# Performance work log

Measured on AMD Instinct MI355X. Metric: run time of the kernel, lower is better.

The kernel has to match this reference:

```python
import math
import jax, jax.numpy as jnp
import numpy as np

L, H, C, HS = 12, 12, 768, 64
V, BS = 50304, 1024
B, T = 2, 1024
FINAL_TH = 0.0005
MIN_KEEP = 64


def _layernorm(x, w, b):
    m = x.mean(-1, keepdims=True)
    v = ((x - m) ** 2).mean(-1, keepdims=True)
    return (x - m) * jax.lax.rsqrt(v + 1e-5) * w + b


def setup_inputs() -> dict:
    key = jax.random.key(0)
    ks = jax.random.split(key, 12)
    std = 0.02
    inp = {
        "idx": jax.random.randint(ks[0], (B, T), 0, V),
        "targets": jax.random.randint(ks[1], (B, T), 0, V),
        # embeddings (wte is tied with lm_head)
        "wte": jax.random.normal(ks[2], (V, C), jnp.float32) * std,
        "wpe": jax.random.normal(ks[3], (BS, C), jnp.float32) * std,
        # stacked per-layer params (leading dim L) -- weights stored (in, out)
        "ln1_w": jnp.ones((L, C), jnp.float32),
        "ln1_b": jnp.zeros((L, C), jnp.float32),
        "attn_w": jax.random.normal(ks[4], (L, C, 3 * C), jnp.float32) * std,
        "attn_b": jnp.zeros((L, 3 * C), jnp.float32),
        "proj_w": jax.random.normal(ks[5], (L, C, C), jnp.float32) * std,
        "proj_b": jnp.zeros((L, C), jnp.float32),
        "ln2_w": jnp.ones((L, C), jnp.float32),
        "ln2_b": jnp.zeros((L, C), jnp.float32),
        "fc_w": jax.random.normal(ks[6], (L, C, 4 * C), jnp.float32) * std,
        "fc_b": jnp.zeros((L, 4 * C), jnp.float32),
        "mlp_w": jax.random.normal(ks[7], (L, 4 * C, C), jnp.float32) * std,
        "mlp_b": jnp.zeros((L, C), jnp.float32),
        # learned thresholds: (layer_idx+1)/n_layer * final_token_threshold
        "thresholds": (jnp.arange(1, L + 1, dtype=jnp.float32) / L) * FINAL_TH,
        "lnf_w": jnp.ones((C,), jnp.float32),
        "lnf_b": jnp.zeros((C,), jnp.float32),
    }
    return inp


def _forward(idx, targets, wte, wpe, ln1_w, ln1_b, attn_w, attn_b, proj_w, proj_b,
             ln2_w, ln2_b, fc_w, fc_b, mlp_w, mlp_b, thresholds, lnf_w, lnf_b):
    Bv, Tv = idx.shape
    x = wte[idx] + wpe[:Tv]  # (B,T,C); dropout=0 -> identity
    causal = jnp.tril(jnp.ones((Tv, Tv), bool))
    protected = jnp.zeros((Bv, Tv), jnp.float32).at[:, -MIN_KEEP:].set(1.0)
    am0 = jnp.ones((Bv, Tv), jnp.float32)

    def block(carry, p):
        x, am = carry
        l1w, l1b, aw, ab, pw, pb, l2w, l2b, fw, fb, mw, mb, th = p
        h = _layernorm(x, l1w, l1b)
        qkv = h @ aw + ab  # (B,T,3C)
        q, k, v = jnp.split(qkv, 3, axis=-1)
        q = q.reshape(Bv, Tv, H, HS).transpose(0, 2, 1, 3)  # (B,H,T,hs)
        k = k.reshape(Bv, Tv, H, HS).transpose(0, 2, 1, 3)
        v = v.reshape(Bv, Tv, H, HS).transpose(0, 2, 1, 3)
        att = jnp.einsum('bhqd,bhkd->bhqk', q, k) / math.sqrt(HS)
        keym = am[:, None, None, :] > 0
        att = jnp.where(causal[None, None] & keym, att, -jnp.inf)
        att = jax.nn.softmax(att, axis=-1)  # attn_dropout=0
        y = jnp.einsum('bhqk,bhkd->bhqd', att, v)
        y = y.transpose(0, 2, 1, 3).reshape(Bv, Tv, C) @ pw + pb  # resid_dropout=0
        x = x + y
        imp = att.mean(axis=(1, 2))  # (B,T): mean over heads then queries
        pm = (imp >= th).astype(x.dtype)  # hard mask
        pm = jnp.where(protected > 0, 1.0, pm)
        cm = am * pm
        x = x * cm[..., None]
        h2 = _layernorm(x, l2w, l2b)
        x = x + (jax.nn.gelu(h2 @ fw + fb, approximate=False) @ mw + mb)
        return (x, cm), None

    params = (ln1_w, ln1_b, attn_w, attn_b, proj_w, proj_b,
              ln2_w, ln2_b, fc_w, fc_b, mlp_w, mlp_b, thresholds)
    (x, am), _ = jax.lax.scan(block, (x, am0), params)
    x = _layernorm(x, lnf_w, lnf_b)
    logits = x @ wte.T  # tied lm_head
    logp = jax.nn.log_softmax(logits, axis=-1)
    nll = -jnp.take_along_axis(logp, targets[..., None], axis=-1)[..., 0]
    valid = targets != -1  # ignore_index=-1
    loss = jnp.where(valid, nll, 0.0).sum() / valid.sum()
    # hard masking => pruning loss is 0, loss == lm_loss
    return logits, loss


def reference(idx, targets, wte, wpe, ln1_w, ln1_b, attn_w, attn_b, proj_w, proj_b,
              ln2_w, ln2_b, fc_w, fc_b, mlp_w, mlp_b, thresholds, lnf_w, lnf_b):
    return _forward(idx, targets, wte, wpe, ln1_w, ln1_b, attn_w, attn_b,
                    proj_w, proj_b, ln2_w, ln2_b, fc_w, fc_b, mlp_w, mlp_b,
                    thresholds, lnf_w, lnf_b)
```

## Files before the change

kernel.cpp:

```cpp
#include <hip/hip_runtime.h>
#include <math.h>


#define LNUM 12
#define HNUM 12
#define CDIM 768
#define VDIM 50304
#define TDIM 1024
#define BDIM 2
#define NROWS 2048
#define LDSK 40

typedef unsigned short u16;
typedef __attribute__((ext_vector_type(8))) short short8;
typedef __attribute__((ext_vector_type(4))) float floatx4;
typedef __attribute__((ext_vector_type(4))) unsigned short ushort4v;
typedef __attribute__((ext_vector_type(8))) unsigned short ushort8v;

__device__ __forceinline__ unsigned short f2bf_rne(float f) {
  unsigned u = __float_as_uint(f);
  u += 0x7fff + ((u >> 16) & 1);
  return (unsigned short)(u >> 16);
}
__device__ __forceinline__ float bf2f(unsigned short h) {
  return __uint_as_float(((unsigned)h) << 16);
}

__device__ __forceinline__ void gload16(const void* g, void* l) {
  __builtin_amdgcn_global_load_lds(
      (const __attribute__((address_space(1))) unsigned int*)g,
      (__attribute__((address_space(3))) unsigned int*)l, 16, 0, 0);
}

__device__ __forceinline__ float bred(float v, int op) {
  __shared__ float red[256];
  const int tid = threadIdx.x;
  red[tid] = v;
  __syncthreads();
#pragma unroll
  for (int s = 128; s > 0; s >>= 1) {
    if (tid < s) {
      float o = red[tid + s];
      red[tid] = op ? fmaxf(red[tid], o) : (red[tid] + o);
    }
    __syncthreads();
  }
  float r = red[0];
  __syncthreads();
  return r;
}

__global__ void k_embed(const int* __restrict__ idx, const float* __restrict__ wte,
                        const float* __restrict__ wpe, float* __restrict__ x,
                        float* __restrict__ am) {
  const int row = blockIdx.x;
  const int t = row & (TDIM - 1);
  const long tok = idx[row];
  const float* src = wte + tok * CDIM;
  const float* pp = wpe + (long)t * CDIM;
  float* dst = x + (long)row * CDIM;
  for (int c = threadIdx.x; c < CDIM; c += 256) dst[c] = src[c] + pp[c];
  if (threadIdx.x == 0) am[row] = 1.0f;
}

__global__ void k_layernorm(const float* __restrict__ in, const float* __restrict__ w,
                            const float* __restrict__ b, float* __restrict__ out) {
  const long row = blockIdx.x;
  const int tid = threadIdx.x;
  const float* xr = in + row * CDIM;
  float v0 = xr[tid], v1 = xr[tid + 256], v2 = xr[tid + 512];
  float mean = bred(v0 + v1 + v2, 0) * (1.0f / CDIM);
  float d0 = v0 - mean, d1 = v1 - mean, d2 = v2 - mean;
  float var = bred(d0 * d0 + d1 * d1 + d2 * d2, 0) * (1.0f / CDIM);
  float inv = 1.0f / sqrtf(var + 1e-5f);
  float* orow = out + row * CDIM;
  orow[tid]       = d0 * inv * w[tid]       + b[tid];
  orow[tid + 256] = d1 * inv * w[tid + 256] + b[tid + 256];
  orow[tid + 512] = d2 * inv * w[tid + 512] + b[tid + 512];
}

__global__ void k_layernorm_sp(const float* __restrict__ in, const float* __restrict__ w,
                               const float* __restrict__ b, u16* __restrict__ ohi,
                               u16* __restrict__ olo) {
  const long row = blockIdx.x;
  const int tid = threadIdx.x;
  const float* xr = in + row * CDIM;
  float v0 = xr[tid], v1 = xr[tid + 256], v2 = xr[tid + 512];
  float mean = bred(v0 + v1 + v2, 0) * (1.0f / CDIM);
  float d0 = v0 - mean, d1 = v1 - mean, d2 = v2 - mean;
  float var = bred(d0 * d0 + d1 * d1 + d2 * d2, 0) * (1.0f / CDIM);
  float inv = 1.0f / sqrtf(var + 1e-5f);
  float o0 = d0 * inv * w[tid]       + b[tid];
  float o1 = d1 * inv * w[tid + 256] + b[tid + 256];
  float o2 = d2 * inv * w[tid + 512] + b[tid + 512];
  u16* hr = ohi + row * CDIM;
  u16* lr = olo + row * CDIM;
  u16 h0 = f2bf_rne(o0), h1 = f2bf_rne(o1), h2 = f2bf_rne(o2);
  hr[tid] = h0;       lr[tid] = f2bf_rne(o0 - bf2f(h0));
  hr[tid + 256] = h1; lr[tid + 256] = f2bf_rne(o1 - bf2f(h1));
  hr[tid + 512] = h2; lr[tid + 512] = f2bf_rne(o2 - bf2f(h2));
}

__global__ void k_wsplit(const float* __restrict__ W, u16* __restrict__ Whi,
                         u16* __restrict__ Wlo, int K, int N, long wstride, long ostride) {
  W += blockIdx.z * wstride;
  Whi += blockIdx.z * ostride;
  Wlo += blockIdx.z * ostride;
  const int n0 = blockIdx.x << 6, k0 = blockIdx.y << 6;
  __shared__ float t[64][65];
  const int tid = threadIdx.x;
  const int cr = tid >> 4;
  const int cc = (tid & 15) << 2;
#pragma unroll
  for (int it = 0; it < 4; ++it) {
    const int r = cr + it * 16;
    float4 v = *(const float4*)(W + (long)(k0 + r) * N + n0 + cc);
    t[r][cc] = v.x; t[r][cc + 1] = v.y; t[r][cc + 2] = v.z; t[r][cc + 3] = v.w;
  }
  __syncthreads();
#pragma unroll
  for (int it = 0; it < 4; ++it) {
    const int n = cr + it * 16;
    ushort4v hv, lv;
#pragma unroll
    for (int j = 0; j < 4; ++j) {
      float f = t[cc + j][n];
      u16 hh = f2bf_rne(f);
      hv[j] = hh;
      lv[j] = f2bf_rne(f - bf2f(hh));
    }
    *(ushort4v*)&Whi[(long)(n0 + n) * K + k0 + cc] = hv;
    *(ushort4v*)&Wlo[(long)(n0 + n) * K + k0 + cc] = lv;
  }
}

__global__ void k_cvt_hi(const float* __restrict__ A, u16* __restrict__ O, long n) {
  long i = ((long)blockIdx.x * 256 + threadIdx.x) * 8;
  if (i >= n) return;
  float4 a = *(const float4*)(A + i);
  float4 b = *(const float4*)(A + i + 4);
  ushort8v o;
  o[0] = f2bf_rne(a.x); o[1] = f2bf_rne(a.y); o[2] = f2bf_rne(a.z); o[3] = f2bf_rne(a.w);
  o[4] = f2bf_rne(b.x); o[5] = f2bf_rne(b.y); o[6] = f2bf_rne(b.z); o[7] = f2bf_rne(b.w);
  *(ushort8v*)&O[i] = o;
}

template <int BT, int ACT, int OSPLIT>
__global__ __launch_bounds__(256) void k_gemm(
    const float* __restrict__ A, const float* __restrict__ B,
    const float* __restrict__ bias, float* __restrict__ C,
    u16* __restrict__ Ohi, u16* __restrict__ Olo,
    int K, int lda, int ldb, int ldc,
    long sAb, long sAh, long sBb, long sBh, long sCb, long sCh,
    int Hb, float alpha, int beta) {
  const int bid = blockIdx.z;
  const int bb = bid / Hb, hh = bid - bb * Hb;
  A += bb * sAb + hh * sAh;
  B += bb * sBb + hh * sBh;
  C += bb * sCb + hh * sCh;
  if (OSPLIT) { Ohi += bb * sCb + hh * sCh; Olo += bb * sCb + hh * sCh; }
  const int m0 = blockIdx.y << 6, n0 = blockIdx.x << 6;
  __shared__ float As[16][68];
  __shared__ float Bs[16][68];
  const int tid = threadIdx.x;
  const int r0 = (tid >> 4) << 2;
  const int c0 = (tid & 15) << 2;
  const int lr = tid >> 2;
  const int lk = (tid & 3) << 2;
  const int bk = tid >> 4;
  const int bn = (tid & 15) << 2;
  float acc[4][4] = {{0.f, 0.f, 0.f, 0.f}, {0.f, 0.f, 0.f, 0.f},
                     {0.f, 0.f, 0.f, 0.f}, {0.f, 0.f, 0.f, 0.f}};
  for (int k0 = 0; k0 < K; k0 += 16) {
    float4 av = *(const float4*)(A + (long)(m0 + lr) * lda + (k0 + lk));
    As[lk][lr] = av.x; As[lk + 1][lr] = av.y; As[lk + 2][lr] = av.z; As[lk + 3][lr] = av.w;
    if (BT) {
      float4 bv = *(const float4*)(B + (long)(n0 + lr) * ldb + (k0 + lk));
      Bs[lk][lr] = bv.x; Bs[lk + 1][lr] = bv.y; Bs[lk + 2][lr] = bv.z; Bs[lk + 3][lr] = bv.w;
    } else {
      *(float4*)&Bs[bk][bn] = *(const float4*)(B + (long)(k0 + bk) * ldb + (n0 + bn));
    }
    __syncthreads();
#pragma unroll
    for (int kk = 0; kk < 16; ++kk) {
      float4 a = *(const float4*)&As[kk][r0];
      float4 bv = *(const float4*)&Bs[kk][c0];
      acc[0][0] += a.x * bv.x; acc[0][1] += a.x * bv.y; acc[0][2] += a.x * bv.z; acc[0][3] += a.x * bv.w;
      acc[1][0] += a.y * bv.x; acc[1][1] += a.y * bv.y; acc[1][2] += a.y * bv.z; acc[1][3] += a.y * bv.w;
      acc[2][0] += a.z * bv.x; acc[2][1] += a.z * bv.y; acc[2][2] += a.z * bv.z; acc[2][3] += a.z * bv.w;
      acc[3][0] += a.w * bv.x; acc[3][1] += a.w * bv.y; acc[3][2] += a.w * bv.z; acc[3][3] += a.w * bv.w;
    }
    __syncthreads();
  }
  float4 bs4 = make_float4(0.f, 0.f, 0.f, 0.f);
  if (bias) bs4 = *(const float4*)(bias + n0 + c0);
#pragma unroll
  for (int i = 0; i < 4; ++i) {
    float* cp = C + (long)(m0 + r0 + i) * ldc + (n0 + c0);
    float4 prev = make_float4(0.f, 0.f, 0.f, 0.f);
    if (beta) prev = *(const float4*)cp;
    float4 o;
    o.x = prev.x + alpha * acc[i][0] + bs4.x;
    o.y = prev.y + alpha * acc[i][1] + bs4.y;
    o.z = prev.z + alpha * acc[i][2] + bs4.z;
    o.w = prev.w + alpha * acc[i][3] + bs4.w;
    if (ACT == 1) {
      o.x = 0.5f * o.x * (1.0f + erff(o.x * 0.70710678118654752f));
      o.y = 0.5f * o.y * (1.0f + erff(o.y * 0.70710678118654752f));
      o.z = 0.5f * o.z * (1.0f + erff(o.z * 0.70710678118654752f));
      o.w = 0.5f * o.w * (1.0f + erff(o.w * 0.70710678118654752f));
    }
    if (OSPLIT) {
      ushort4v hv, lv;
      hv[0] = f2bf_rne(o.x); lv[0] = f2bf_rne(o.x - bf2f(hv[0]));
      hv[1] = f2bf_rne(o.y); lv[1] = f2bf_rne(o.y - bf2f(hv[1]));
      hv[2] = f2bf_rne(o.z); lv[2] = f2bf_rne(o.z - bf2f(hv[2]));
      hv[3] = f2bf_rne(o.w); lv[3] = f2bf_rne(o.w - bf2f(hv[3]));
      *(ushort4v*)(Ohi + (long)(m0 + r0 + i) * ldc + (n0 + c0)) = hv;
      *(ushort4v*)(Olo + (long)(m0 + r0 + i) * ldc + (n0 + c0)) = lv;
    } else {
      *(float4*)cp = o;
    }
  }
}

template <int TERMS, int ACT, int OUTMODE, int GS>
__global__ __launch_bounds__(256) void k_gemm_bt(
    const u16* __restrict__ Ahi, const u16* __restrict__ Alo,
    const u16* __restrict__ Bhi, const u16* __restrict__ Blo,
    const float* __restrict__ bias, float* __restrict__ C,
    u16* __restrict__ Ohi, u16* __restrict__ Olo,
    int K, int lda, int ldb, int ldc,
    long sAb, long sAh, long sBb, long sBh, long sCb, long sCh,
    int Hb, float alpha, int beta) {
  const int bz = blockIdx.z;
  const int bb = bz / Hb, hh = bz - bb * Hb;
  Ahi += bb * sAb + hh * sAh;
  Bhi += bb * sBb + hh * sBh;
  if (TERMS > 1) {
    Alo += bb * sAb + hh * sAh;
    Blo += bb * sBb + hh * sBh;
  }
  if (OUTMODE != 1) C += bb * sCb + hh * sCh;
  if (OUTMODE >= 1) { Ohi += bb * sCb + hh * sCh; Olo += bb * sCb + hh * sCh; }
  const int m0 = (GS ? blockIdx.x : blockIdx.y) << 7;
  const int n0 = (GS ? blockIdx.y : blockIdx.x) << 7;
  __shared__ u16 sm[(TERMS > 1 ? 4 : 2) * 4096];
  u16* sAhi = sm;
  u16* sAlo = sm + 4096;
  u16* sBhi = sm + (TERMS > 1 ? 2 : 1) * 4096;
  u16* sBlo = sBhi + 4096;
  const int tid = threadIdx.x;
  const int lane = tid & 63, wave = tid >> 6;
  const int wm = (wave & 1) << 6, wn = (wave >> 1) << 6;
  const int fr = lane & 15, fk = (lane >> 4) << 3;
  const int sr = lane >> 2;
  const int sc = (lane & 3) << 3;
  const long arow = (long)(m0 + wave * 32 + sr);
  const long brow = (long)(n0 + wave * 32 + sr);
  const int lbase = wave * 1024;

  floatx4 acc[4][4];
#pragma unroll
  for (int i = 0; i < 4; ++i)
#pragma unroll
    for (int j = 0; j < 4; ++j) acc[i][j] = (floatx4)(0.0f);

  for (int k0 = 0; k0 < K; k0 += 32) {
    {
      const u16* ga = Ahi + arow * lda + k0 + sc;
      const u16* gb = Bhi + brow * ldb + k0 + sc;
      gload16(ga, &sAhi[lbase]);
      gload16(ga + (long)16 * lda, &sAhi[lbase + 512]);
      gload16(gb, &sBhi[lbase]);
      gload16(gb + (long)16 * ldb, &sBhi[lbase + 512]);
      if (TERMS > 1) {
        const u16* ga2 = Alo + arow * lda + k0 + sc;
        const u16* gb2 = Blo + brow * ldb + k0 + sc;
        gload16(ga2, &sAlo[lbase]);
        gload16(ga2 + (long)16 * lda, &sAlo[lbase + 512]);
        gload16(gb2, &sBlo[lbase]);
        gload16(gb2 + (long)16 * ldb, &sBlo[lbase + 512]);
      }
    }
    __syncthreads();
    short8 ah[4], bh[4], al[4], bl[4];
#pragma unroll
    for (int i = 0; i < 4; ++i) {
      ah[i] = *(const short8*)&sAhi[(wm + i * 16 + fr) * 32 + fk];
      bh[i] = *(const short8*)&sBhi[(wn + i * 16 + fr) * 32 + fk];
      if (TERMS > 1) {
        al[i] = *(const short8*)&sAlo[(wm + i * 16 + fr) * 32 + fk];
        bl[i] = *(const short8*)&sBlo[(wn + i * 16 + fr) * 32 + fk];
      }
    }
#pragma unroll
    for (int i = 0; i < 4; ++i)
#pragma unroll
      for (int j = 0; j < 4; ++j) {
        acc[i][j] = __builtin_amdgcn_mfma_f32_16x16x32_bf16(ah[i], bh[j], acc[i][j], 0, 0, 0);
        if (TERMS > 1) {
          acc[i][j] = __builtin_amdgcn_mfma_f32_16x16x32_bf16(ah[i], bl[j], acc[i][j], 0, 0, 0);
          acc[i][j] = __builtin_amdgcn_mfma_f32_16x16x32_bf16(al[i], bh[j], acc[i][j], 0, 0, 0);
        }
      }
    __syncthreads();
  }
  const int er = (lane >> 4) << 2, ec = lane & 15;
#pragma unroll
  for (int j = 0; j < 4; ++j) {
    const int col = n0 + wn + j * 16 + ec;
    const float bsv = bias ? bias[col] : 0.0f;
#pragma unroll
    for (int i = 0; i < 4; ++i) {
      const long rbase = (long)(m0 + wm + i * 16 + er);
#pragma unroll
      for (int r = 0; r < 4; ++r) {
        const long off = (rbase + r) * ldc + col;
        float o = alpha * acc[i][j][r] + bsv;
        if (beta) o += C[off];
        if (ACT == 1) o = 0.5f * o * (1.0f + erff(o * 0.70710678118654752f));
        if (OUTMODE != 1) C[off] = o;
        if (OUTMODE >= 1) {
          u16 hv = f2bf_rne(o);
          Ohi[off] = hv;
          Olo[off] = f2bf_rne(o - bf2f(hv));
        }
      }
    }
  }
}

template <int BT, int TERMS, int ACT, int GS>
__global__ __launch_bounds__(256) void k_gemm_mfma(
    const float* __restrict__ A, const float* __restrict__ B,
    const float* __restrict__ bias, float* __restrict__ C,
    int K, int lda, int ldb, int ldc, int beta) {
  const int m0 = (GS ? blockIdx.x : blockIdx.y) << 7;
  const int n0 = (GS ? blockIdx.y : blockIdx.x) << 7;
  __shared__ unsigned short sm[(TERMS > 1 ? 4 : 2) * 128 * LDSK];
  unsigned short* As_hi = sm;
  unsigned short* As_lo = (TERMS > 1) ? (sm + 128 * LDSK) : sm;
  unsigned short* Bs_hi = sm + (TERMS > 1 ? 2 : 1) * 128 * LDSK;
  unsigned short* Bs_lo = (TERMS > 1) ? (Bs_hi + 128 * LDSK) : Bs_hi;
  const int tid = threadIdx.x;
  const int lane = tid & 63, wave = tid >> 6;
  const int wm = (wave & 1) << 6, wn = (wave >> 1) << 6;
  const int fr = lane & 15;
  const int fk = (lane >> 4) << 3;
  const int ar = tid >> 1, ak = (tid & 1) << 4;
  const int bn = tid & 31, bk = (tid >> 5) << 2;

  floatx4 acc[4][4];
#pragma unroll
  for (int i = 0; i < 4; ++i)
#pragma unroll
    for (int j = 0; j < 4; ++j) acc[i][j] = (floatx4)(0.0f);

  for (int k0 = 0; k0 < K; k0 += 32) {
    {
      const float* ap = A + (long)(m0 + ar) * lda + (k0 + ak);
      float4 f0 = *(const float4*)(ap);
      float4 f1 = *(const float4*)(ap + 4);
      float4 f2 = *(const float4*)(ap + 8);
      float4 f3 = *(const float4*)(ap + 12);
      float va[16] = {f0.x, f0.y, f0.z, f0.w, f1.x, f1.y, f1.z, f1.w,
                      f2.x, f2.y, f2.z, f2.w, f3.x, f3.y, f3.z, f3.w};
      ushort8v h0, h1, l0, l1;
#pragma unroll
      for (int i = 0; i < 8; ++i) {
        unsigned short hA = f2bf_rne(va[i]);
        unsigned short hB = f2bf_rne(va[8 + i]);
        h0[i] = hA; h1[i] = hB;
        if (TERMS > 1) {
          l0[i] = f2bf_rne(va[i] - bf2f(hA));
          l1[i] = f2bf_rne(va[8 + i] - bf2f(hB));
        }
      }
      *(ushort8v*)&As_hi[ar * LDSK + ak]     = h0;
      *(ushort8v*)&As_hi[ar * LDSK + ak + 8] = h1;
      if (TERMS > 1) {
        *(ushort8v*)&As_lo[ar * LDSK + ak]     = l0;
        *(ushort8v*)&As_lo[ar * LDSK + ak + 8] = l1;
      }
    }
    if (BT) {
      const float* bp = B + (long)(n0 + ar) * ldb + (k0 + ak);
      float4 f0 = *(const float4*)(bp);
      float4 f1 = *(const float4*)(bp + 4);
      float4 f2 = *(const float4*)(bp + 8);
      float4 f3 = *(const float4*)(bp + 12);
      float vb[16] = {f0.x, f0.y, f0.z, f0.w, f1.x, f1.y, f1.z, f1.w,
                      f2.x, f2.y, f2.z, f2.w, f3.x, f3.y, f3.z, f3.w};
      ushort8v h0, h1, l0, l1;
#pragma unroll
      for (int i = 0; i < 8; ++i) {
        unsigned short hA = f2bf_rne(vb[i]);
        unsigned short hB = f2bf_rne(vb[8 + i]);
        h0[i] = hA; h1[i] = hB;
        if (TERMS > 1) {
          l0[i] = f2bf_rne(vb[i] - bf2f(hA));
          l1[i] = f2bf_rne(vb[8 + i] - bf2f(hB));
        }
      }
      *(ushort8v*)&Bs_hi[ar * LDSK + ak]     = h0;
      *(ushort8v*)&Bs_hi[ar * LDSK + ak + 8] = h1;
      if (TERMS > 1) {
        *(ushort8v*)&Bs_lo[ar * LDSK + ak]     = l0;
        *(ushort8v*)&Bs_lo[ar * LDSK + ak + 8] = l1;
      }
    } else {
      float bvv[4][4];
#pragma unroll
      for (int j = 0; j < 4; ++j)
#pragma unroll
        for (int r = 0; r < 4; ++r)
          bvv[j][r] = B[(long)(k0 + bk + r) * ldb + (n0 + bn + 32 * j)];
#pragma unroll
      for (int j = 0; j < 4; ++j) {
        ushort4v hv, lv;
#pragma unroll
        for (int r = 0; r < 4; ++r) {
          unsigned short hh = f2bf_rne(bvv[j][r]);
          hv[r] = hh;
          if (TERMS > 1) lv[r] = f2bf_rne(bvv[j][r] - bf2f(hh));
        }
        *(ushort4v*)&Bs_hi[(bn + 32 * j) * LDSK + bk] = hv;
        if (TERMS > 1) *(ushort4v*)&Bs_lo[(bn + 32 * j) * LDSK + bk] = lv;
      }
    }
    __syncthreads();
    short8 a_hi[4], a_lo[4], b_hi[4], b_lo[4];
#pragma unroll
    for (int i = 0; i < 4; ++i) {
      a_hi[i] = *(const short8*)&As_hi[(wm + i * 16 + fr) * LDSK + fk];
      b_hi[i] = *(const short8*)&Bs_hi[(wn + i * 16 + fr) * LDSK + fk];
      if (TERMS > 1) {
        a_lo[i] = *(const short8*)&As_lo[(wm + i * 16 + fr) * LDSK + fk];
        b_lo[i] = *(const short8*)&Bs_lo[(wn + i * 16 + fr) * LDSK + fk];
      }
    }
#pragma unroll
    for (int i = 0; i < 4; ++i)
#pragma unroll
      for (int j = 0; j < 4; ++j) {
        acc[i][j] = __builtin_amdgcn_mfma_f32_16x16x32_bf16(a_hi[i], b_hi[j], acc[i][j], 0, 0, 0);
        if (TERMS > 1) {
          acc[i][j] = __builtin_amdgcn_mfma_f32_16x16x32_bf16(a_hi[i], b_lo[j], acc[i][j], 0, 0, 0);
          acc[i][j] = __builtin_amdgcn_mfma_f32_16x16x32_bf16(a_lo[i], b_hi[j], acc[i][j], 0, 0, 0);
        }
      }
    __syncthreads();
  }
  const int er = (lane >> 4) << 2;
  const int ec = lane & 15;
#pragma unroll
  for (int j = 0; j < 4; ++j) {
    const int col = n0 + wn + j * 16 + ec;
    const float bsv = bias ? bias[col] : 0.0f;
#pragma unroll
    for (int i = 0; i < 4; ++i) {
#pragma unroll
      for (int r = 0; r < 4; ++r) {
        float* cp = C + (long)(m0 + wm + i * 16 + er + r) * ldc + col;
        float o = acc[i][j][r] + bsv + (beta ? *cp : 0.0f);
        if (ACT == 1) o = 0.5f * o * (1.0f + erff(o * 0.70710678118654752f));
        *cp = o;
      }
    }
  }
}

__global__ void k_softmax(float* __restrict__ att, const float* __restrict__ am) {
  const int q = blockIdx.x;
  const int bh = blockIdx.y;
  const int b = bh / HNUM;
  float* row = att + ((long)bh * TDIM + q) * TDIM;
  const float* amr = am + b * TDIM;
  const int tid = threadIdx.x;
  float lv[4];
  bool valid[4];
  float mx = -INFINITY;
#pragma unroll
  for (int i = 0; i < 4; ++i) {
    const int k = tid + (i << 8);
    const bool ok = (k <= q) && (amr[k] > 0.0f);
    valid[i] = ok;
    lv[i] = ok ? row[k] : -INFINITY;
    mx = fmaxf(mx, lv[i]);
  }
  mx = bred(mx, 1);
  float sum = 0.f;
#pragma unroll
  for (int i = 0; i < 4; ++i) {
    lv[i] = valid[i] ? expf(lv[i] - mx) : 0.0f;
    sum += lv[i];
  }
  sum = bred(sum, 0);
  const float inv = sum > 0.f ? 1.0f / sum : 0.0f;
#pragma unroll
  for (int i = 0; i < 4; ++i) row[tid + (i << 8)] = lv[i] * inv;
}

__global__ void k_impsum(const float* __restrict__ att, float* __restrict__ imp) {
  const int h = blockIdx.x >> 2, qc = blockIdx.x & 3;
  const int b = blockIdx.z;
  const int k = (blockIdx.y << 8) + threadIdx.x;
  const float* base = att + (((long)(b * HNUM + h) * TDIM) + (qc << 8)) * TDIM + k;
  float s = 0.f;
#pragma unroll 4
  for (int q = 0; q < 256; ++q) s += base[(long)q * TDIM];
  atomicAdd(&imp[b * TDIM + k], s);
}

__global__ void k_mask(const float* __restrict__ imp, const float* __restrict__ thp,
                       float* __restrict__ am, float* __restrict__ x) {
  const int row = blockIdx.x;
  const int t = row & (TDIM - 1);
  const float impv = imp[row] * (1.0f / (HNUM * TDIM));
  float pm = (impv >= *thp) ? 1.0f : 0.0f;
  if (t >= TDIM - 64) pm = 1.0f;
  const float cm = am[row] * pm;
  float* xr = x + (long)row * CDIM;
  const int tid = threadIdx.x;
  xr[tid] *= cm;
  xr[tid + 256] *= cm;
  xr[tid + 512] *= cm;
  if (tid == 0) am[row] = cm;
}

__global__ void k_lossrow(const float* __restrict__ logits, const int* __restrict__ tgt,
                          float* __restrict__ nll) {
  const int row = blockIdx.x;
  const float* lr = logits + (long)row * VDIM;
  const int tid = threadIdx.x;
  float mx = -INFINITY;
  for (int k = tid; k < VDIM; k += 256) mx = fmaxf(mx, lr[k]);
  mx = bred(mx, 1);
  float s = 0.f;
  for (int k = tid; k < VDIM; k += 256) s += expf(lr[k] - mx);
  s = bred(s, 0);
  if (tid == 0) {
    const int t = tgt[row];
    nll[row] = (t != -1) ? -(lr[t] - mx - logf(s)) : 0.0f;
  }
}

__global__ void k_lossfinal(const float* __restrict__ nll, const int* __restrict__ tgt,
                            float* __restrict__ out) {
  const int tid = threadIdx.x;
  float s = 0.f, cnt = 0.f;
  for (int r = tid; r < NROWS; r += 256) {
    s += nll[r];
    cnt += (tgt[r] != -1) ? 1.f : 0.f;
  }
  s = bred(s, 0);
  cnt = bred(cnt, 0);
  if (tid == 0) out[0] = s / cnt;
}

extern "C" void kernel_launch(void* const* d_in, const int* in_sizes, int n_in,
                              void* d_out, int out_size, void* d_ws, size_t ws_size,
                              hipStream_t stream) {
  (void)in_sizes; (void)n_in; (void)out_size;
  const int* idx      = (const int*)d_in[0];
  const int* targets  = (const int*)d_in[1];
  const float* wte    = (const float*)d_in[2];
  const float* wpe    = (const float*)d_in[3];
  const float* ln1_w  = (const float*)d_in[4];
  const float* ln1_b  = (const float*)d_in[5];
  const float* attn_w = (const float*)d_in[6];
  const float* attn_b = (const float*)d_in[7];
  const float* proj_w = (const float*)d_in[8];
  const float* proj_b = (const float*)d_in[9];
  const float* ln2_w  = (const float*)d_in[10];
  const float* ln2_b  = (const float*)d_in[11];
  const float* fc_w   = (const float*)d_in[12];
  const float* fc_b   = (const float*)d_in[13];
  const float* mlp_w  = (const float*)d_in[14];
  const float* mlp_b  = (const float*)d_in[15];
  const float* thres  = (const float*)d_in[16];
  const float* lnf_w  = (const float*)d_in[17];
  const float* lnf_b  = (const float*)d_in[18];
  float* logits = (float*)d_out;
  float* loss = logits + (long)NROWS * VDIM;

  const long F_X   = (long)NROWS * CDIM;
  const long F_QKV = (long)NROWS * 3 * CDIM;
  const long F_ATT = (long)BDIM * HNUM * TDIM * TDIM;
  const long U_H   = (long)NROWS * CDIM;
  const long U_ACT = (long)NROWS * 4 * CDIM;
  const long U_QKV = F_QKV;
  const long WA = (long)CDIM * 3 * CDIM;
  const long WP = (long)CDIM * CDIM;
  const long WF = (long)CDIM * 4 * CDIM;
  const long WM = (long)4 * CDIM * CDIM;
  const long WPL = WA + WP + WF + WM;
  const long U_W   = (long)LNUM * WPL;
  const long U_WTE = (long)VDIM * CDIM;
  const unsigned long long need =
      4ull * (F_X + F_QKV + F_ATT + 3 * NROWS) +
      2ull * (4 * U_H + 2 * U_ACT + 2 * U_QKV + 2 * U_W + U_WTE);

  float* x   = (float*)d_ws;
  float* qkv = x + F_X;

  if (ws_size >= need) {
    float* att = qkv + F_QKV;
    float* am  = att + F_ATT;
    float* imp = am + NROWS;
    float* nll = imp + NROWS;
    u16* h_hi   = (u16*)(nll + NROWS);
    u16* h_lo   = h_hi + U_H;
    u16* y_hi   = h_lo + U_H;
    u16* y_lo   = y_hi + U_H;
    u16* act_hi = y_lo + U_H;
    u16* act_lo = act_hi + U_ACT;
    u16* qkv_hi = act_lo + U_ACT;
    u16* qkv_lo = qkv_hi + U_QKV;
    u16* w_hi   = qkv_lo + U_QKV;
    u16* w_lo   = w_hi + U_W;
    u16* wte_h  = w_lo + U_W;

    k_wsplit<<<dim3(3 * CDIM / 64, CDIM / 64, LNUM), 256, 0, stream>>>(
        attn_w, w_hi, w_lo, CDIM, 3 * CDIM, WA, WPL);
    k_wsplit<<<dim3(CDIM / 64, CDIM / 64, LNUM), 256, 0, stream>>>(
        proj_w, w_hi + WA, w_lo + WA, CDIM, CDIM, WP, WPL);
    k_wsplit<<<dim3(4 * CDIM / 64, CDIM / 64, LNUM), 256, 0, stream>>>(
        fc_w, w_hi + WA + WP, w_lo + WA + WP, CDIM, 4 * CDIM, WF, WPL);
    k_wsplit<<<dim3(CDIM / 64, 4 * CDIM / 64, LNUM), 256, 0, stream>>>(
        mlp_w, w_hi + WA + WP + WF, w_lo + WA + WP + WF, 4 * CDIM, CDIM, WM, WPL);
    k_cvt_hi<<<(unsigned)((U_WTE / 8 + 255) / 256), 256, 0, stream>>>(wte, wte_h, U_WTE);

    k_embed<<<NROWS, 256, 0, stream>>>(idx, wte, wpe, x, am);

    for (int l = 0; l < LNUM; ++l) {
      const u16* wa_h = w_hi + (long)l * WPL;
      const u16* wa_l = w_lo + (long)l * WPL;
      const u16* wp_h = wa_h + WA;
      const u16* wp_l = wa_l + WA;
      const u16* wf_h = wp_h + WP;
      const u16* wf_l = wp_l + WP;
      const u16* wm_h = wf_h + WF;
      const u16* wm_l = wf_l + WF;

      k_layernorm_sp<<<NROWS, 256, 0, stream>>>(x, ln1_w + l * CDIM, ln1_b + l * CDIM, h_hi, h_lo);
      k_gemm_bt<3, 0, 2, 0><<<dim3(18, 16), 256, 0, stream>>>(
          h_hi, h_lo, wa_h, wa_l, attn_b + (long)l * 3 * CDIM, qkv, qkv_hi, qkv_lo,
          768, 768, 768, 2304, 0, 0, 0, 0, 0, 0, 1, 1.0f, 0);
      k_gemm_bt<3, 0, 0, 0><<<dim3(8, 8, BDIM * HNUM), 256, 0, stream>>>(
          qkv_hi, qkv_lo, qkv_hi + CDIM, qkv_lo + CDIM, nullptr, att, nullptr, nullptr,
          64, 2304, 2304, 1024,
          (long)TDIM * 3 * CDIM, 64, (long)TDIM * 3 * CDIM, 64,
          (long)HNUM * TDIM * TDIM, (long)TDIM * TDIM, HNUM, 0.125f, 0);
      k_softmax<<<dim3(TDIM, BDIM * HNUM), 256, 0, stream>>>(att, am);
      hipMemsetAsync(imp, 0, NROWS * sizeof(float), stream);
      k_impsum<<<dim3(HNUM * 4, 4, BDIM), 256, 0, stream>>>(att, imp);
      k_gemm<0, 0, 1><<<dim3(1, 16, BDIM * HNUM), 256, 0, stream>>>(
          att, qkv + 2 * CDIM, nullptr, nullptr, y_hi, y_lo,
          1024, 1024, 2304, 768,
          (long)HNUM * TDIM * TDIM, (long)TDIM * TDIM, (long)TDIM * 3 * CDIM, 64,
          (long)TDIM * CDIM, 64, HNUM, 1.0f, 0);
      k_gemm_bt<3, 0, 0, 0><<<dim3(6, 16), 256, 0, stream>>>(
          y_hi, y_lo, wp_h, wp_l, proj_b + (long)l * CDIM, x, nullptr, nullptr,
          768, 768, 768, 768, 0, 0, 0, 0, 0, 0, 1, 1.0f, 1);
      k_mask<<<NROWS, 256, 0, stream>>>(imp, thres + l, am, x);
      k_layernorm_sp<<<NROWS, 256, 0, stream>>>(x, ln2_w + l * CDIM, ln2_b + l * CDIM, h_hi, h_lo);
      k_gemm_bt<3, 1, 1, 0><<<dim3(24, 16), 256, 0, stream>>>(
          h_hi, h_lo, wf_h, wf_l, fc_b + (long)l * 4 * CDIM, nullptr, act_hi, act_lo,
          768, 768, 768, 3072, 0, 0, 0, 0, 0, 0, 1, 1.0f, 0);
      k_gemm_bt<3, 0, 0, 0><<<dim3(6, 16), 256, 0, stream>>>(
          act_hi, act_lo, wm_h, wm_l, mlp_b + (long)l * CDIM, x, nullptr, nullptr,
          3072, 3072, 3072, 768, 0, 0, 0, 0, 0, 0, 1, 1.0f, 1);
    }

    k_layernorm_sp<<<NROWS, 256, 0, stream>>>(x, lnf_w, lnf_b, h_hi, h_lo);
    k_gemm_bt<1, 0, 0, 1><<<dim3(16, 393), 256, 0, stream>>>(
        h_hi, nullptr, wte_h, nullptr, nullptr, logits, nullptr, nullptr,
        768, 768, 768, VDIM, 0, 0, 0, 0, 0, 0, 1, 1.0f, 0);
    k_lossrow<<<NROWS, 256, 0, stream>>>(logits, targets, nll);
    k_lossfinal<<<1, 256, 0, stream>>>(nll, targets, loss);
  } else {
    float* h    = qkv;
    h    = x + F_X;
    qkv  = h + F_X;
    float* att  = qkv + F_QKV;
    float* ybuf = att + F_ATT;
    float* act  = ybuf + F_X;
    float* am   = act + (long)NROWS * 4 * CDIM;
    float* imp  = am + NROWS;
    float* nll  = imp + NROWS;

    k_embed<<<NROWS, 256, 0, stream>>>(idx, wte, wpe, x, am);
    for (int l = 0; l < LNUM; ++l) {
      k_layernorm<<<NROWS, 256, 0, stream>>>(x, ln1_w + l * CDIM, ln1_b + l * CDIM, h);
      k_gemm_mfma<0, 3, 0, 0><<<dim3(18, 16), 256, 0, stream>>>(
          h, attn_w + (long)l * CDIM * 3 * CDIM, attn_b + (long)l * 3 * CDIM, qkv,
          768, 768, 2304, 2304, 0);
      k_gemm<1, 0, 0><<<dim3(16, 16, 24), 256, 0, stream>>>(
          qkv, qkv + CDIM, nullptr, att, nullptr, nullptr,
          64, 2304, 2304, 1024,
          (long)TDIM * 3 * CDIM, 64, (long)TDIM * 3 * CDIM, 64,
          (long)HNUM * TDIM * TDIM, (long)TDIM * TDIM, HNUM, 0.125f, 0);
      k_softmax<<<dim3(TDIM, BDIM * HNUM), 256, 0, stream>>>(att, am);
      hipMemsetAsync(imp, 0, NROWS * sizeof(float), stream);
      k_impsum<<<dim3(HNUM * 4, 4, BDIM), 256, 0, stream>>>(att, imp);
      k_gemm<0, 0, 0><<<dim3(1, 16, 24), 256, 0, stream>>>(
          att, qkv + 2 * CDIM, nullptr, ybuf, nullptr, nullptr,
          1024, 1024, 2304, 768,
          (long)HNUM * TDIM * TDIM, (long)TDIM * TDIM, (long)TDIM * 3 * CDIM, 64,
          (long)TDIM * CDIM, 64, HNUM, 1.0f, 0);
      k_gemm_mfma<0, 3, 0, 0><<<dim3(6, 16), 256, 0, stream>>>(
          ybuf, proj_w + (long)l * CDIM * CDIM, proj_b + (long)l * CDIM, x,
          768, 768, 768, 768, 1);
      k_mask<<<NROWS, 256, 0, stream>>>(imp, thres + l, am, x);
      k_layernorm<<<NROWS, 256, 0, stream>>>(x, ln2_w + l * CDIM, ln2_b + l * CDIM, h);
      k_gemm_mfma<0, 3, 1, 0><<<dim3(24, 16), 256, 0, stream>>>(
          h, fc_w + (long)l * CDIM * 4 * CDIM, fc_b + (long)l * 4 * CDIM, act,
          768, 768, 3072, 3072, 0);
      k_gemm_mfma<0, 3, 0, 0><<<dim3(6, 16), 256, 0, stream>>>(
          act, mlp_w + (long)l * 4 * CDIM * CDIM, mlp_b + (long)l * CDIM, x,
          3072, 3072, 768, 768, 1);
    }
    k_layernorm<<<NROWS, 256, 0, stream>>>(x, lnf_w, lnf_b, h);
    k_gemm_mfma<1, 1, 0, 1><<<dim3(16, 393), 256, 0, stream>>>(
        h, wte, nullptr, logits, 768, 768, 768, VDIM, 0);
    k_lossrow<<<NROWS, 256, 0, stream>>>(logits, targets, nll);
    k_lossfinal<<<1, 256, 0, stream>>>(nll, targets, loss);
  }
}
```

Baseline: 7.199 ms.

## Split-K with atomics for small GEMMs, XCD block swizzle, online-softmax loss

The QKV, proj and MLP-down GEMMs are now split along K across blockIdx.z and accumulate into fp32 output with atomicAdd. Bias is added only by the first split, and QKV is zeroed beforehand and then split into hi/lo bf16 by a new kernel. A flat-index swizzle remaps workgroups so neighbouring tiles land on the same XCD, and the loss row kernel uses a single-pass online max/sum with float4 loads. The aim is more occupancy on small-grid GEMMs, better L2 locality and fewer logit passes, at the cost of atomic traffic, an extra memset and split kernel, and a nondeterministic summation order.

```diff
diff --git a/kernel.cpp b/kernel.cpp
--- a/kernel.cpp
+++ b/kernel.cpp
@@ -143,6 +143,20 @@
   o[0] = f2bf_rne(a.x); o[1] = f2bf_rne(a.y); o[2] = f2bf_rne(a.z); o[3] = f2bf_rne(a.w);
   o[4] = f2bf_rne(b.x); o[5] = f2bf_rne(b.y); o[6] = f2bf_rne(b.z); o[7] = f2bf_rne(b.w);
   *(ushort8v*)&O[i] = o;
+}
+
+__global__ void k_split2(const float* __restrict__ A, u16* __restrict__ Ohi,
+                         u16* __restrict__ Olo, long n) {
+  long i = ((long)blockIdx.x * 256 + threadIdx.x) * 4;
+  if (i >= n) return;
+  float4 a = *(const float4*)(A + i);
+  ushort4v hv, lv;
+  hv[0] = f2bf_rne(a.x); lv[0] = f2bf_rne(a.x - bf2f(hv[0]));
+  hv[1] = f2bf_rne(a.y); lv[1] = f2bf_rne(a.y - bf2f(hv[1]));
+  hv[2] = f2bf_rne(a.z); lv[2] = f2bf_rne(a.z - bf2f(hv[2]));
+  hv[3] = f2bf_rne(a.w); lv[3] = f2bf_rne(a.w - bf2f(hv[3]));
+  *(ushort4v*)&Ohi[i] = hv;
+  *(ushort4v*)&Olo[i] = lv;
 }
 
 template <int BT, int ACT, int OSPLIT>
@@ -224,7 +238,7 @@
   }
 }
 
-template <int TERMS, int ACT, int OUTMODE, int GS>
+template <int TERMS, int ACT, int OUTMODE, int GS, int ATOMIC, int XCD>
 __global__ __launch_bounds__(256) void k_gemm_bt(
     const u16* __restrict__ Ahi, const u16* __restrict__ Alo,
     const u16* __restrict__ Bhi, const u16* __restrict__ Blo,
@@ -232,7 +246,7 @@
     u16* __restrict__ Ohi, u16* __restrict__ Olo,
     int K, int lda, int ldb, int ldc,
     long sAb, long sAh, long sBb, long sBh, long sCb, long sCh,
-    int Hb, float alpha, int beta) {
+    int Hb, float alpha, int beta, int swzq) {
   const int bz = blockIdx.z;
   const int bb = bz / Hb, hh = bz - bb * Hb;
   Ahi += bb * sAb + hh * sAh;
@@ -243,8 +257,15 @@
   }
   if (OUTMODE != 1) C += bb * sCb + hh * sCh;
   if (OUTMODE >= 1) { Ohi += bb * sCb + hh * sCh; Olo += bb * sCb + hh * sCh; }
-  const int m0 = (GS ? blockIdx.x : blockIdx.y) << 7;
-  const int n0 = (GS ? blockIdx.y : blockIdx.x) << 7;
+  int bx = blockIdx.x, by = blockIdx.y;
+  if (XCD) {
+    const int flat = by * gridDim.x + bx;
+    const int wg = (flat & 7) * swzq + (flat >> 3);
+    bx = wg % gridDim.x;
+    by = wg / gridDim.x;
+  }
+  const int m0 = (GS ? bx : by) << 7;
+  const int n0 = (GS ? by : bx) << 7;
   __shared__ u16 sm[(TERMS > 1 ? 4 : 2) * 4096];
   u16* sAhi = sm;
   u16* sAlo = sm + 4096;
@@ -310,7 +331,7 @@
 #pragma unroll
   for (int j = 0; j < 4; ++j) {
     const int col = n0 + wn + j * 16 + ec;
-    const float bsv = bias ? bias[col] : 0.0f;
+    const float bsv = (bias && (!ATOMIC || hh == 0)) ? bias[col] : 0.0f;
 #pragma unroll
     for (int i = 0; i < 4; ++i) {
       const long rbase = (long)(m0 + wm + i * 16 + er);
@@ -318,13 +339,17 @@
       for (int r = 0; r < 4; ++r) {
         const long off = (rbase + r) * ldc + col;
         float o = alpha * acc[i][j][r] + bsv;
-        if (beta) o += C[off];
-        if (ACT == 1) o = 0.5f * o * (1.0f + erff(o * 0.70710678118654752f));
-        if (OUTMODE != 1) C[off] = o;
-        if (OUTMODE >= 1) {
-          u16 hv = f2bf_rne(o);
-          Ohi[off] = hv;
-          Olo[off] = f2bf_rne(o - bf2f(hv));
+        if (ATOMIC) {
+          atomicAdd(&C[off], o);
+        } else {
+          if (beta) o += C[off];
+          if (ACT == 1) o = 0.5f * o * (1.0f + erff(o * 0.70710678118654752f));
+          if (OUTMODE != 1) C[off] = o;
+          if (OUTMODE >= 1) {
+            u16 hv = f2bf_rne(o);
+            Ohi[off] = hv;
+            Olo[off] = f2bf_rne(o - bf2f(hv));
+          }
         }
       }
     }
@@ -534,15 +559,29 @@
   const int row = blockIdx.x;
   const float* lr = logits + (long)row * VDIM;
   const int tid = threadIdx.x;
-  float mx = -INFINITY;
-  for (int k = tid; k < VDIM; k += 256) mx = fmaxf(mx, lr[k]);
-  mx = bred(mx, 1);
-  float s = 0.f;
-  for (int k = tid; k < VDIM; k += 256) s += expf(lr[k] - mx);
-  s = bred(s, 0);
+  float mx = -INFINITY, s = 0.f;
+  for (int k = tid * 4; k < VDIM; k += 1024) {
+    float4 v = *(const float4*)(lr + k);
+    float m4 = fmaxf(fmaxf(v.x, v.y), fmaxf(v.z, v.w));
+    if (m4 > mx) { s *= expf(mx - m4); mx = m4; }
+    s += expf(v.x - mx) + expf(v.y - mx) + expf(v.z - mx) + expf(v.w - mx);
+  }
+  __shared__ float sm_[256], ss_[256];
+  sm_[tid] = mx; ss_[tid] = s;
+  __syncthreads();
+#pragma unroll
+  for (int st = 128; st > 0; st >>= 1) {
+    if (tid < st) {
+      float m2 = sm_[tid + st], s2 = ss_[tid + st];
+      float M = fmaxf(sm_[tid], m2);
+      ss_[tid] = ss_[tid] * expf(sm_[tid] - M) + s2 * expf(m2 - M);
+      sm_[tid] = M;
+    }
+    __syncthreads();
+  }
   if (tid == 0) {
     const int t = tgt[row];
-    nll[row] = (t != -1) ? -(lr[t] - mx - logf(s)) : 0.0f;
+    nll[row] = (t != -1) ? -(lr[t] - sm_[0] - logf(ss_[0])) : 0.0f;
   }
 }
 
@@ -645,14 +684,16 @@
       const u16* wm_l = wf_l + WF;
 
       k_layernorm_sp<<<NROWS, 256, 0, stream>>>(x, ln1_w + l * CDIM, ln1_b + l * CDIM, h_hi, h_lo);
-      k_gemm_bt<3, 0, 2, 0><<<dim3(18, 16), 256, 0, stream>>>(
-          h_hi, h_lo, wa_h, wa_l, attn_b + (long)l * 3 * CDIM, qkv, qkv_hi, qkv_lo,
-          768, 768, 768, 2304, 0, 0, 0, 0, 0, 0, 1, 1.0f, 0);
-      k_gemm_bt<3, 0, 0, 0><<<dim3(8, 8, BDIM * HNUM), 256, 0, stream>>>(
+      hipMemsetAsync(qkv, 0, F_QKV * sizeof(float), stream);
+      k_gemm_bt<3, 0, 0, 1, 1, 1><<<dim3(16, 18, 2), 256, 0, stream>>>(
+          h_hi, h_lo, wa_h, wa_l, attn_b + (long)l * 3 * CDIM, qkv, nullptr, nullptr,
+          384, 768, 768, 2304, 0, 384, 0, 384, 0, 0, 2, 1.0f, 0, 36);
+      k_split2<<<(unsigned)(F_QKV / 4 / 256), 256, 0, stream>>>(qkv, qkv_hi, qkv_lo, F_QKV);
+      k_gemm_bt<3, 0, 0, 0, 0, 0><<<dim3(8, 8, BDIM * HNUM), 256, 0, stream>>>(
           qkv_hi, qkv_lo, qkv_hi + CDIM, qkv_lo + CDIM, nullptr, att, nullptr, nullptr,
           64, 2304, 2304, 1024,
           (long)TDIM * 3 * CDIM, 64, (long)TDIM * 3 * CDIM, 64,
-          (long)HNUM * TDIM * TDIM, (long)TDIM * TDIM, HNUM, 0.125f, 0);
+          (long)HNUM * TDIM * TDIM, (long)TDIM * TDIM, HNUM, 0.125f, 0, 0);
       k_softmax<<<dim3(TDIM, BDIM * HNUM), 256, 0, stream>>>(att, am);
       hipMemsetAsync(imp, 0, NROWS * sizeof(float), stream);
       k_impsum<<<dim3(HNUM * 4, 4, BDIM), 256, 0, stream>>>(att, imp);
@@ -661,30 +702,29 @@
           1024, 1024, 2304, 768,
           (long)HNUM * TDIM * TDIM, (long)TDIM * TDIM, (long)TDIM * 3 * CDIM, 64,
           (long)TDIM * CDIM, 64, HNUM, 1.0f, 0);
-      k_gemm_bt<3, 0, 0, 0><<<dim3(6, 16), 256, 0, stream>>>(
+      k_gemm_bt<3, 0, 0, 1, 1, 1><<<dim3(16, 6, 4), 256, 0, stream>>>(
           y_hi, y_lo, wp_h, wp_l, proj_b + (long)l * CDIM, x, nullptr, nullptr,
-          768, 768, 768, 768, 0, 0, 0, 0, 0, 0, 1, 1.0f, 1);
+          192, 768, 768, 768, 0, 192, 0, 192, 0, 0, 4, 1.0f, 0, 12);
       k_mask<<<NROWS, 256, 0, stream>>>(imp, thres + l, am, x);
       k_layernorm_sp<<<NROWS, 256, 0, stream>>>(x, ln2_w + l * CDIM, ln2_b + l * CDIM, h_hi, h_lo);
-      k_gemm_bt<3, 1, 1, 0><<<dim3(24, 16), 256, 0, stream>>>(
+      k_gemm_bt<3, 1, 1, 1, 0, 1><<<dim3(16, 24), 256, 0, stream>>>(
           h_hi, h_lo, wf_h, wf_l, fc_b + (long)l * 4 * CDIM, nullptr, act_hi, act_lo,
-          768, 768, 768, 3072, 0, 0, 0, 0, 0, 0, 1, 1.0f, 0);
-      k_gemm_bt<3, 0, 0, 0><<<dim3(6, 16), 256, 0, stream>>>(
+          768, 768, 768, 3072, 0, 0, 0, 0, 0, 0, 1, 1.0f, 0, 48);
+      k_gemm_bt<3, 0, 0, 1, 1, 1><<<dim3(16, 6, 4), 256, 0, stream>>>(
           act_hi, act_lo, wm_h, wm_l, mlp_b + (long)l * CDIM, x, nullptr, nullptr,
-          3072, 3072, 3072, 768, 0, 0, 0, 0, 0, 0, 1, 1.0f, 1);
+          768, 3072, 3072, 768, 0, 768, 0, 768, 0, 0, 4, 1.0f, 0, 12);
     }
 
     k_layernorm_sp<<<NROWS, 256, 0, stream>>>(x, lnf_w, lnf_b, h_hi, h_lo);
-    k_gemm_bt<1, 0, 0, 1><<<dim3(16, 393), 256, 0, stream>>>(
+    k_gemm_bt<1, 0, 0, 1, 0, 1><<<dim3(16, 393), 256, 0, stream>>>(
         h_hi, nullptr, wte_h, nullptr, nullptr, logits, nullptr, nullptr,
-        768, 768, 768, VDIM, 0, 0, 0, 0, 0, 0, 1, 1.0f, 0);
+        768, 768, 768, VDIM, 0, 0, 0, 0, 0, 0, 1, 1.0f, 0, 786);
     k_lossrow<<<NROWS, 256, 0, stream>>>(logits, targets, nll);
     k_lossfinal<<<1, 256, 0, stream>>>(nll, targets, loss);
   } else {
-    float* h    = qkv;
-    h    = x + F_X;
-    qkv  = h + F_X;
-    float* att  = qkv + F_QKV;
+    float* h    = x + F_X;
+    float* qkv2 = h + F_X;
+    float* att  = qkv2 + F_QKV;
     float* ybuf = att + F_ATT;
     float* act  = ybuf + F_X;
     float* am   = act + (long)NROWS * 4 * CDIM;
@@ -695,10 +735,10 @@
     for (int l = 0; l < LNUM; ++l) {
       k_layernorm<<<NROWS, 256, 0, stream>>>(x, ln1_w + l * CDIM, ln1_b + l * CDIM, h);
       k_gemm_mfma<0, 3, 0, 0><<<dim3(18, 16), 256, 0, stream>>>(
-          h, attn_w + (long)l * CDIM * 3 * CDIM, attn_b + (long)l * 3 * CDIM, qkv,
+          h, attn_w + (long)l * CDIM * 3 * CDIM, attn_b + (long)l * 3 * CDIM, qkv2,
           768, 768, 2304, 2304, 0);
       k_gemm<1, 0, 0><<<dim3(16, 16, 24), 256, 0, stream>>>(
-          qkv, qkv + CDIM, nullptr, att, nullptr, nullptr,
+          qkv2, qkv2 + CDIM, nullptr, att, nullptr, nullptr,
           64, 2304, 2304, 1024,
           (long)TDIM * 3 * CDIM, 64, (long)TDIM * 3 * CDIM, 64,
           (long)HNUM * TDIM * TDIM, (long)TDIM * TDIM, HNUM, 0.125f, 0);
@@ -706,7 +746,7 @@
       hipMemsetAsync(imp, 0, NROWS * sizeof(float), stream);
       k_impsum<<<dim3(HNUM * 4, 4, BDIM), 256, 0, stream>>>(att, imp);
       k_gemm<0, 0, 0><<<dim3(1, 16, 24), 256, 0, stream>>>(
-          att, qkv + 2 * CDIM, nullptr, ybuf, nullptr, nullptr,
+          att, qkv2 + 2 * CDIM, nullptr, ybuf, nullptr, nullptr,
           1024, 1024, 2304, 768,
           (long)HNUM * TDIM * TDIM, (long)TDIM * TDIM, (long)TDIM * 3 * CDIM, 64,
           (long)TDIM * CDIM, 64, HNUM, 1.0f, 0);
```

New measurement: 6.065 ms. 15.8% less time.
